# Optimization experiments

Hardware: AMD Instinct MI355X
Metric: run time of the kernel (lower is better)

The kernel has to match this reference:

```python
import jax, jax.numpy as jnp
import numpy as np

N_NODES = 100000
N_EDGES = 1600000
D_IN = 64
D_OUT = 64


def setup_inputs() -> dict:
    key = jax.random.key(0)
    k1, k2, k3, k4 = jax.random.split(key, 4)
    feat = jax.random.normal(k1, (N_NODES, D_IN), dtype=jnp.float32)
    edge_src = jax.random.randint(k2, (N_EDGES,), 0, N_NODES, dtype=jnp.int64)
    edge_dst = jax.random.randint(k3, (N_EDGES,), 0, N_NODES, dtype=jnp.int64)
    # xavier_uniform with gain for relu (sqrt(2)) on [out, in] Linear weight
    gain = float(np.sqrt(2.0))
    limit = gain * float(np.sqrt(6.0 / (D_IN + D_OUT)))
    fc_weight = jax.random.uniform(k4, (D_OUT, D_IN), dtype=jnp.float32,
                                   minval=-limit, maxval=limit)
    return {"feat": feat, "edge_src": edge_src, "edge_dst": edge_dst,
            "fc_weight": fc_weight}


def reference(feat, edge_src, edge_dst, fc_weight):
    # SDDMM: edge score a_e = <h_src, h_dst>  (fn.u_dot_v)
    h_src = feat[edge_src]                      # [E, d]
    h_dst = feat[edge_dst]                      # [E, d]
    a = jnp.sum(h_src * h_dst, axis=-1, keepdims=True)  # [E, 1]
    # SpMM: neigh[v] = sum_{(u->v)} h_u * a_e  (u_mul_e + sum)
    m = h_src * a                               # [E, d]
    neigh = jax.ops.segment_sum(m, edge_dst, num_segments=feat.shape[0])  # [N, d]
    # Linear without bias: y = neigh @ W.T
    return neigh @ fc_weight.T
```

## Files before the change

kernel.cpp:

```cpp
#include <hip/hip_runtime.h>

#define N_NODES 100000
#define N_EDGES 1600000
#define D 64
#define NB 782
#define CAP 3072
#define EPB 8192
#define NPART ((N_EDGES + EPB - 1) / EPB)
#define RSH 14

typedef unsigned short ushort_t;
typedef unsigned int uint_t;

__device__ __forceinline__ ushort_t f2bf(float f) {
    uint_t u = __float_as_uint(f);
    u += 0x7FFF + ((u >> 16) & 1);
    return (ushort_t)(u >> 16);
}

__global__ __launch_bounds__(256) void repack_init(const float* __restrict__ feat,
                                                   ushort_t* __restrict__ featb,
                                                   int* __restrict__ gcur) {
    const int tid = blockIdx.x * 256 + threadIdx.x;
    if (tid < NB) gcur[tid] = tid * CAP;
    const int base = tid * 16;
    if (base >= N_NODES * D) return;
    const float4* f4 = (const float4*)(feat + base);
    ushort4* o4 = (ushort4*)(featb + base);
#pragma unroll
    for (int j = 0; j < 4; ++j) {
        const float4 v = f4[j];
        o4[j] = make_ushort4(f2bf(v.x), f2bf(v.y), f2bf(v.z), f2bf(v.w));
    }
}

__global__ __launch_bounds__(1024) void partition(const int* __restrict__ esrc,
                                                  const int* __restrict__ edst,
                                                  int* __restrict__ gcur,
                                                  int* __restrict__ slab) {
    __shared__ int stage[EPB];
    __shared__ ushort_t bkt16[EPB];
    __shared__ int cnt[NB];
    __shared__ int cur[NB];
    __shared__ int gb[NB];
    __shared__ int s[1024];
    const int t = threadIdx.x;
    const int base = blockIdx.x * EPB;
    const int n = min(EPB, N_EDGES - base);

    if (t < NB) cnt[t] = 0;
    __syncthreads();
    for (int i = t; i < n; i += 1024)
        atomicAdd(&cnt[edst[base + i] >> 7], 1);
    __syncthreads();
    const int v = (t < NB) ? cnt[t] : 0;
    s[t] = v;
    __syncthreads();
    for (int off = 1; off < 1024; off <<= 1) {
        const int x = (t >= off) ? s[t - off] : 0;
        __syncthreads();
        s[t] += x;
        __syncthreads();
    }
    if (t < NB) {
        const int excl = s[t] - v;
        cur[t] = excl;
        gb[t] = (v ? atomicAdd(&gcur[t], v) : 0) - excl;
    }
    __syncthreads();
    for (int i = t; i < n; i += 1024) {
        const int d = edst[base + i];
        const int bkt = d >> 7;
        const int pos = atomicAdd(&cur[bkt], 1);
        stage[pos] = ((d & 127) << 17) | esrc[base + i];
        bkt16[pos] = (ushort_t)bkt;
    }
    __syncthreads();
    for (int i = t; i < n; i += 1024) {
        const int bkt = bkt16[i];
        const int gp = gb[bkt] + i;
        if (gp < (bkt + 1) * CAP)
            slab[gp] = stage[i];
    }
}

template<int CTRL>
__device__ __forceinline__ float fadd_dpp(float x) {
    const int r = __builtin_amdgcn_update_dpp(0, __float_as_int(x), CTRL, 0xF, 0xF, true);
    return x + __int_as_float(r);
}
__device__ __forceinline__ float red8(float p) {
    p = fadd_dpp<0xB1>(p);
    p = fadd_dpp<0x4E>(p);
    p = fadd_dpp<0x141>(p);
    return p;
}

__device__ __forceinline__ float cvt_dot(const uint4 u, const float* __restrict__ h,
                                         float* __restrict__ g) {
    g[0] = __uint_as_float(u.x << 16); g[1] = __uint_as_float(u.x & 0xFFFF0000u);
    g[2] = __uint_as_float(u.y << 16); g[3] = __uint_as_float(u.y & 0xFFFF0000u);
    g[4] = __uint_as_float(u.z << 16); g[5] = __uint_as_float(u.z & 0xFFFF0000u);
    g[6] = __uint_as_float(u.w << 16); g[7] = __uint_as_float(u.w & 0xFFFF0000u);
    float p = 0.f;
#pragma unroll
    for (int k = 0; k < 8; ++k) p += g[k] * h[k];
    return p;
}

__global__ __launch_bounds__(512) void fused_spmm(const float4* __restrict__ feat4,
                                                  const uint4* __restrict__ featb4,
                                                  const int* __restrict__ slab,
                                                  const int* __restrict__ gcur,
                                                  float4* __restrict__ neigh4) {
    __shared__ int seA[CAP];
    __shared__ int seB[CAP];
    __shared__ int cnt[1024];
    __shared__ int cur[1024];
    __shared__ int rowoff[129];
    __shared__ int s[512];
    const int t = threadIdx.x;
    const int b = blockIdx.x;
    const int nbase = b << 7;
    const int nb_nodes = min(128, N_NODES - nbase);
    const int sbase = b * CAP;
    const int ne = min(gcur[b] - sbase, CAP);

    for (int i = t; i < ne; i += 512) seA[i] = slab[sbase + i];
    cnt[t] = 0; cnt[t + 512] = 0;
    __syncthreads();
    for (int i = t; i < ne; i += 512) {
        const int pk = seA[i];
        atomicAdd(&cnt[((pk >> 17) << 3) | ((pk & 0x1FFFF) >> RSH)], 1);
    }
    __syncthreads();
    const int v0 = cnt[2 * t], v1 = cnt[2 * t + 1];
    const int sum = v0 + v1;
    s[t] = sum;
    __syncthreads();
    for (int off = 1; off < 512; off <<= 1) {
        const int x = (t >= off) ? s[t - off] : 0;
        __syncthreads();
        s[t] += x;
        __syncthreads();
    }
    const int excl = s[t] - sum;
    cur[2 * t] = excl;
    cur[2 * t + 1] = excl + v0;
    __syncthreads();
    if (t < 128) rowoff[t] = cur[t << 3];
    if (t == 0) rowoff[128] = ne;
    __syncthreads();
    for (int i = t; i < ne; i += 512) {
        const int pk = seA[i];
        const int key = ((pk >> 17) << 3) | ((pk & 0x1FFFF) >> RSH);
        const int pos = atomicAdd(&cur[key], 1);
        seB[pos] = pk & 0x1FFFF;
    }
    __syncthreads();

    const int slot = t >> 3;
    const int l = t & 7;
#pragma unroll
    for (int ln0 = 0; ln0 < 128; ln0 += 64) {
        const int ln = ln0 + slot;
        if (ln >= nb_nodes) continue;
        const int nidx = nbase + ln;
        float h[8];
        {
            const float4 ha = feat4[nidx * 16 + 2 * l];
            const float4 hb = feat4[nidx * 16 + 2 * l + 1];
            h[0] = ha.x; h[1] = ha.y; h[2] = ha.z; h[3] = ha.w;
            h[4] = hb.x; h[5] = hb.y; h[6] = hb.z; h[7] = hb.w;
        }
        float acc[8];
#pragma unroll
        for (int k = 0; k < 8; ++k) acc[k] = 0.f;

        int e = rowoff[ln];
        const int e1 = rowoff[ln + 1];
        const int nq = (e1 - e) >> 2;
        if (nq > 0) {
            int s0 = seB[e], s1 = seB[e + 1], s2 = seB[e + 2], s3 = seB[e + 3];
            uint4 u0 = featb4[s0 * 8 + l];
            uint4 u1 = featb4[s1 * 8 + l];
            uint4 u2 = featb4[s2 * 8 + l];
            uint4 u3 = featb4[s3 * 8 + l];
            for (int q = 1; q < nq; ++q) {
                const int eb = e + q * 4;
                const int t0 = seB[eb], t1 = seB[eb + 1];
                const int t2 = seB[eb + 2], t3 = seB[eb + 3];
                const uint4 w0 = featb4[t0 * 8 + l];
                const uint4 w1 = featb4[t1 * 8 + l];
                const uint4 w2 = featb4[t2 * 8 + l];
                const uint4 w3 = featb4[t3 * 8 + l];
                float g0[8], g1[8], g2[8], g3[8];
                float p0 = cvt_dot(u0, h, g0);
                float p1 = cvt_dot(u1, h, g1);
                float p2 = cvt_dot(u2, h, g2);
                float p3 = cvt_dot(u3, h, g3);
                p0 = red8(p0); p1 = red8(p1); p2 = red8(p2); p3 = red8(p3);
#pragma unroll
                for (int k = 0; k < 8; ++k)
                    acc[k] += g0[k] * p0 + g1[k] * p1 + g2[k] * p2 + g3[k] * p3;
                u0 = w0; u1 = w1; u2 = w2; u3 = w3;
            }
            {
                float g0[8], g1[8], g2[8], g3[8];
                float p0 = cvt_dot(u0, h, g0);
                float p1 = cvt_dot(u1, h, g1);
                float p2 = cvt_dot(u2, h, g2);
                float p3 = cvt_dot(u3, h, g3);
                p0 = red8(p0); p1 = red8(p1); p2 = red8(p2); p3 = red8(p3);
#pragma unroll
                for (int k = 0; k < 8; ++k)
                    acc[k] += g0[k] * p0 + g1[k] * p1 + g2[k] * p2 + g3[k] * p3;
            }
            e += nq * 4;
        }
        for (; e < e1; ++e) {
            const uint4 u0 = featb4[seB[e] * 8 + l];
            float g0[8];
            float p0 = red8(cvt_dot(u0, h, g0));
#pragma unroll
            for (int k = 0; k < 8; ++k) acc[k] += g0[k] * p0;
        }
        neigh4[nidx * 16 + 2 * l]     = make_float4(acc[0], acc[1], acc[2], acc[3]);
        neigh4[nidx * 16 + 2 * l + 1] = make_float4(acc[4], acc[5], acc[6], acc[7]);
    }
}

__global__ __launch_bounds__(256) void gemm_inplace(float* __restrict__ out,
                                                    const float* __restrict__ W) {
    __shared__ float WT[64][68];
    __shared__ float nT[64][132];
    const int t = threadIdx.x;

    const float4* W4 = (const float4*)W;
#pragma unroll
    for (int j = 0; j < 4; ++j) {
        const int f = t + j * 256;
        const int o = f >> 4;
        const int i4 = (f & 15) * 4;
        const float4 w = W4[f];
        WT[i4 + 0][o] = w.x;
        WT[i4 + 1][o] = w.y;
        WT[i4 + 2][o] = w.z;
        WT[i4 + 3][o] = w.w;
    }

    const int base = blockIdx.x * 128;
    const int rows = min(128, N_NODES - base);
    const float4* O4 = (const float4*)(out + (long)base * D);
#pragma unroll
    for (int j = 0; j < 8; ++j) {
        const int f = t + j * 256;
        const int r = f >> 4;
        const int i4 = (f & 15) * 4;
        if (r < rows) {
            const float4 x = O4[f];
            nT[i4 + 0][r] = x.x;
            nT[i4 + 1][r] = x.y;
            nT[i4 + 2][r] = x.z;
            nT[i4 + 3][r] = x.w;
        }
    }
    __syncthreads();

    const int c4 = (t & 15) * 4;
    const int r0 = (t >> 4) * 8;
    float acc[8][4];
#pragma unroll
    for (int r = 0; r < 8; ++r)
#pragma unroll
        for (int c = 0; c < 4; ++c) acc[r][c] = 0.f;

    for (int i = 0; i < 64; ++i) {
        const float4 w = *(const float4*)&WT[i][c4];
        const float4 ra = *(const float4*)&nT[i][r0];
        const float4 rb = *(const float4*)&nT[i][r0 + 4];
        const float wv[4] = {w.x, w.y, w.z, w.w};
        const float rv[8] = {ra.x, ra.y, ra.z, ra.w, rb.x, rb.y, rb.z, rb.w};
#pragma unroll
        for (int r = 0; r < 8; ++r)
#pragma unroll
            for (int c = 0; c < 4; ++c) acc[r][c] += rv[r] * wv[c];
    }

#pragma unroll
    for (int r = 0; r < 8; ++r) {
        const int rr = r0 + r;
        if (rr < rows)
            *(float4*)&out[(long)(base + rr) * D + c4] =
                make_float4(acc[r][0], acc[r][1], acc[r][2], acc[r][3]);
    }
}

extern "C" void kernel_launch(void* const* d_in, const int* in_sizes, int n_in,
                              void* d_out, int out_size, void* d_ws, size_t ws_size,
                              hipStream_t stream) {
    const float* feat = (const float*)d_in[0];
    const int*   esrc = (const int*)d_in[1];
    const int*   edst = (const int*)d_in[2];
    const float* W    = (const float*)d_in[3];
    float* out = (float*)d_out;

    char* ws = (char*)d_ws;
    ushort_t* featb = (ushort_t*)(ws);
    int* slab = (int*)(ws + 12800000);
    int* gcur = (int*)(ws + 12800000 + (size_t)NB * CAP * 4);

    repack_init<<<(N_NODES * D / 16 + 255) / 256, 256, 0, stream>>>(feat, featb, gcur);
    partition<<<NPART, 1024, 0, stream>>>(esrc, edst, gcur, slab);
    fused_spmm<<<NB, 512, 0, stream>>>((const float4*)feat, (const uint4*)featb,
                                       slab, gcur, (float4*)out);
    gemm_inplace<<<(N_NODES + 127) / 128, 256, 0, stream>>>(out, W);
}
```

Baseline: 163.8 us.

## Fuse the linear projection into the SpMM kernel via shared-memory aggregated rows

The separate GEMM kernel is removed. Each SpMM block now writes its 128 aggregated node rows into a shared-memory tile that overlays the dead edge buffers, then multiplies that tile by W and writes the final output directly. This removes a kernel launch and the global round trip of the intermediate neigh array. In exchange, W is read from global/L1 by every thread instead of being staged transposed in LDS, and the shared-memory overlay aliasing must be correct.

Result: slower. 512.5 us (+212.9%).

```diff
diff --git a/kernel.cpp b/kernel.cpp
--- a/kernel.cpp
+++ b/kernel.cpp
@@ -108,17 +108,30 @@
     return p;
 }
 
-__global__ __launch_bounds__(512) void fused_spmm(const float4* __restrict__ feat4,
-                                                  const uint4* __restrict__ featb4,
-                                                  const int* __restrict__ slab,
-                                                  const int* __restrict__ gcur,
-                                                  float4* __restrict__ neigh4) {
-    __shared__ int seA[CAP];
-    __shared__ int seB[CAP];
-    __shared__ int cnt[1024];
-    __shared__ int cur[1024];
-    __shared__ int rowoff[129];
-    __shared__ int s[512];
+#define SMEM_BYTES 47632
+#define OFF_ROW 12288
+#define OFF_SEA 12816
+#define OFF_CNT 25104
+#define OFF_CUR 29200
+#define OFF_S   33296
+#define OFF_HN  12816
+
+__global__ __launch_bounds__(512) void fused_spmm_gemm(
+        const float4* __restrict__ feat4,
+        const uint4* __restrict__ featb4,
+        const int* __restrict__ slab,
+        const int* __restrict__ gcur,
+        const float* __restrict__ W,
+        float4* __restrict__ out4) {
+    __shared__ __align__(16) char smem[SMEM_BYTES];
+    int* seB    = (int*)(smem);
+    int* rowoff = (int*)(smem + OFF_ROW);
+    int* seA    = (int*)(smem + OFF_SEA);
+    int* cnt    = (int*)(smem + OFF_CNT);
+    int* cur    = (int*)(smem + OFF_CUR);
+    int* s      = (int*)(smem + OFF_S);
+    float (*hN)[68] = (float(*)[68])(smem + OFF_HN);
+
     const int t = threadIdx.x;
     const int b = blockIdx.x;
     const int nbase = b << 7;
@@ -225,74 +238,42 @@
 #pragma unroll
             for (int k = 0; k < 8; ++k) acc[k] += g0[k] * p0;
         }
-        neigh4[nidx * 16 + 2 * l]     = make_float4(acc[0], acc[1], acc[2], acc[3]);
-        neigh4[nidx * 16 + 2 * l + 1] = make_float4(acc[4], acc[5], acc[6], acc[7]);
-    }
-}
-
-__global__ __launch_bounds__(256) void gemm_inplace(float* __restrict__ out,
-                                                    const float* __restrict__ W) {
-    __shared__ float WT[64][68];
-    __shared__ float nT[64][132];
-    const int t = threadIdx.x;
-
-    const float4* W4 = (const float4*)W;
-#pragma unroll
-    for (int j = 0; j < 4; ++j) {
-        const int f = t + j * 256;
-        const int o = f >> 4;
-        const int i4 = (f & 15) * 4;
-        const float4 w = W4[f];
-        WT[i4 + 0][o] = w.x;
-        WT[i4 + 1][o] = w.y;
-        WT[i4 + 2][o] = w.z;
-        WT[i4 + 3][o] = w.w;
-    }
-
-    const int base = blockIdx.x * 128;
-    const int rows = min(128, N_NODES - base);
-    const float4* O4 = (const float4*)(out + (long)base * D);
-#pragma unroll
-    for (int j = 0; j < 8; ++j) {
-        const int f = t + j * 256;
-        const int r = f >> 4;
-        const int i4 = (f & 15) * 4;
-        if (r < rows) {
-            const float4 x = O4[f];
-            nT[i4 + 0][r] = x.x;
-            nT[i4 + 1][r] = x.y;
-            nT[i4 + 2][r] = x.z;
-            nT[i4 + 3][r] = x.w;
-        }
-    }
-    __syncthreads();
-
-    const int c4 = (t & 15) * 4;
-    const int r0 = (t >> 4) * 8;
-    float acc[8][4];
-#pragma unroll
-    for (int r = 0; r < 8; ++r)
-#pragma unroll
-        for (int c = 0; c < 4; ++c) acc[r][c] = 0.f;
-
-    for (int i = 0; i < 64; ++i) {
-        const float4 w = *(const float4*)&WT[i][c4];
-        const float4 ra = *(const float4*)&nT[i][r0];
-        const float4 rb = *(const float4*)&nT[i][r0 + 4];
-        const float wv[4] = {w.x, w.y, w.z, w.w};
-        const float rv[8] = {ra.x, ra.y, ra.z, ra.w, rb.x, rb.y, rb.z, rb.w};
-#pragma unroll
-        for (int r = 0; r < 8; ++r)
-#pragma unroll
-            for (int c = 0; c < 4; ++c) acc[r][c] += rv[r] * wv[c];
-    }
-
-#pragma unroll
-    for (int r = 0; r < 8; ++r) {
-        const int rr = r0 + r;
-        if (rr < rows)
-            *(float4*)&out[(long)(base + rr) * D + c4] =
-                make_float4(acc[r][0], acc[r][1], acc[r][2], acc[r][3]);
+        *(float4*)&hN[ln][8 * l]     = make_float4(acc[0], acc[1], acc[2], acc[3]);
+        *(float4*)&hN[ln][8 * l + 4] = make_float4(acc[4], acc[5], acc[6], acc[7]);
+    }
+    __syncthreads();
+
+    {
+        const float4* W4 = (const float4*)W;
+        const int c4 = (t & 15) * 4;
+        const int r0 = (t >> 4) * 4;
+        float a[4][4];
+#pragma unroll
+        for (int r = 0; r < 4; ++r)
+#pragma unroll
+            for (int c = 0; c < 4; ++c) a[r][c] = 0.f;
+
+        for (int i4 = 0; i4 < 16; ++i4) {
+            const float4 w0 = W4[(c4 + 0) * 16 + i4];
+            const float4 w1 = W4[(c4 + 1) * 16 + i4];
+            const float4 w2 = W4[(c4 + 2) * 16 + i4];
+            const float4 w3 = W4[(c4 + 3) * 16 + i4];
+#pragma unroll
+            for (int r = 0; r < 4; ++r) {
+                const float4 x = *(const float4*)&hN[r0 + r][i4 * 4];
+                a[r][0] += x.x * w0.x + x.y * w0.y + x.z * w0.z + x.w * w0.w;
+                a[r][1] += x.x * w1.x + x.y * w1.y + x.z * w1.z + x.w * w1.w;
+                a[r][2] += x.x * w2.x + x.y * w2.y + x.z * w2.z + x.w * w2.w;
+                a[r][3] += x.x * w3.x + x.y * w3.y + x.z * w3.z + x.w * w3.w;
+            }
+        }
+#pragma unroll
+        for (int r = 0; r < 4; ++r) {
+            const int rr = r0 + r;
+            if (rr < nb_nodes)
+                out4[(long)(nbase + rr) * 16 + (t & 15)] =
+                    make_float4(a[r][0], a[r][1], a[r][2], a[r][3]);
+        }
     }
 }
 
@@ -312,7 +293,6 @@
 
     repack_init<<<(N_NODES * D / 16 + 255) / 256, 256, 0, stream>>>(feat, featb, gcur);
     partition<<<NPART, 1024, 0, stream>>>(esrc, edst, gcur, slab);
-    fused_spmm<<<NB, 512, 0, stream>>>((const float4*)feat, (const uint4*)featb,
-                                       slab, gcur, (float4*)out);
-    gemm_inplace<<<(N_NODES + 127) / 128, 256, 0, stream>>>(out, W);
-}
+    fused_spmm_gemm<<<NB, 512, 0, stream>>>((const float4*)feat, (const uint4*)featb,
+                                            slab, gcur, W, (float4*)out);
+}
```
